# Kernel optimization log

Hardware: AMD Instinct MI355X
Metric: run time of the kernel (lower is better)

## Reference

```python
import jax, jax.numpy as jnp
import numpy as np

N = 100000
E = 800000
D_IN = 128
D_HID = 128
D_EMB = 128
D_OUT = 2


def setup_inputs() -> dict:
    key = jax.random.key(0)
    ks = jax.random.split(key, 16)
    x = jax.random.normal(ks[0], (N, D_IN), dtype=jnp.float32)
    edge_index = jax.random.randint(ks[1], (2, E), 0, N, dtype=jnp.int64)

    def lin(k, d_out, d_in, scale):
        return jax.random.normal(k, (d_out, d_in), dtype=jnp.float32) * scale

    s1 = 1.0 / np.sqrt(D_IN)
    s2 = 1.0 / np.sqrt(D_HID)
    s3 = 1.0 / np.sqrt(D_EMB)
    return {
        "x": x,
        "edge_index": edge_index,
        # layer 1: in -> hidden  (lin_l has bias, lin_r no bias, as in PyG SAGEConv)
        "Wl1": lin(ks[2], D_HID, D_IN, s1), "bl1": jnp.zeros((D_HID,), jnp.float32),
        "Wr1": lin(ks[3], D_HID, D_IN, s1),
        # layer 2: hidden -> hidden
        "Wl2": lin(ks[4], D_HID, D_HID, s2), "bl2": jnp.zeros((D_HID,), jnp.float32),
        "Wr2": lin(ks[5], D_HID, D_HID, s2),
        # layer 3: hidden -> embedding
        "Wl3": lin(ks[6], D_EMB, D_HID, s2), "bl3": jnp.zeros((D_EMB,), jnp.float32),
        "Wr3": lin(ks[7], D_EMB, D_HID, s2),
        # output head: embedding -> output (bias)
        "Wo": lin(ks[8], D_OUT, D_EMB, s3), "bo": jnp.zeros((D_OUT,), jnp.float32),
    }


def _sage_conv(x, src, dst, Wl, bl, Wr):
    # mean-aggregate neighbor (source) features onto destination nodes
    msg = x[src]                                             # [E, d]
    agg = jax.ops.segment_sum(msg, dst, num_segments=N)      # [N, d]
    deg = jax.ops.segment_sum(jnp.ones((src.shape[0],), x.dtype), dst, num_segments=N)
    agg = agg / jnp.maximum(deg, 1.0)[:, None]
    # out = lin_l(agg) + lin_r(x)
    return agg @ Wl.T + bl + x @ Wr.T


def reference(x, edge_index, Wl1, bl1, Wr1, Wl2, bl2, Wr2, Wl3, bl3, Wr3, Wo, bo):
    src, dst = edge_index[0], edge_index[1]
    h = jax.nn.relu(_sage_conv(x, src, dst, Wl1, bl1, Wr1))   # dropout is identity in eval
    h = jax.nn.relu(_sage_conv(h, src, dst, Wl2, bl2, Wr2))
    h = _sage_conv(h, src, dst, Wl3, bl3, Wr3)                # no relu on last conv
    return h @ Wo.T + bo                                      # [N, D_OUT]
```

## Files before the change

kernel.cpp:

```cpp
#include <hip/hip_runtime.h>
#include <stdint.h>

typedef unsigned int u32;
typedef unsigned short u16;
typedef __bf16 bf16x8 __attribute__((ext_vector_type(8)));
typedef float floatx4 __attribute__((ext_vector_type(4)));
typedef u32 u32x4 __attribute__((ext_vector_type(4)));
typedef float floatx4f __attribute__((ext_vector_type(4)));
typedef float floatx4v __attribute__((ext_vector_type(4)));
typedef float floatx16 __attribute__((ext_vector_type(16)));
typedef float floatx4b __attribute__((ext_vector_type(4)));
typedef float floatx4c __attribute__((ext_vector_type(4)));
typedef float floatx4d __attribute__((ext_vector_type(4)));
typedef float floatx4e __attribute__((ext_vector_type(4)));

__device__ __forceinline__ u16 f2b(float f) {
    u32 u = __builtin_bit_cast(u32, f);
    u32 r = u + 0x7FFFu + ((u >> 16) & 1u);
    return (u16)(r >> 16);
}
__device__ __forceinline__ float lo2f(u32 u) { return __builtin_bit_cast(float, u << 16); }
__device__ __forceinline__ float hi2f(u32 u) { return __builtin_bit_cast(float, u & 0xFFFF0000u); }

__device__ __forceinline__ void self_detect(const int* ei, const u32* xw, int& is64, int& isbf) {
    int lane = threadIdx.x & 63;
    int v = ei ? ei[2 * lane + 1] : 0;
    unsigned long long b1 = __ballot(v == 0);
    u32 w = xw ? xw[lane] : 0;
    u32 e = (w >> 7) & 0xFF;
    int plaus = (e == 0) || (e >= 90 && e <= 140);
    unsigned long long b2 = __ballot(plaus);
    is64 = (b1 == ~0ULL) ? 1 : 0;
    isbf = (b2 == ~0ULL) ? 1 : 0;
}

__device__ __forceinline__ float load_f(const void* __restrict__ p, int isbf, size_t i) {
    if (isbf) {
        u16 s = ((const u16*)p)[i];
        return __builtin_bit_cast(float, ((u32)s) << 16);
    }
    return ((const float*)p)[i];
}

#define CH 4096
#define CAPB 3072

__global__ __launch_bounds__(1024) void front_kernel(
    const void* __restrict__ xraw, const int* __restrict__ ei, int E, int N, int cvb,
    u32* __restrict__ xb, int* __restrict__ gcur, u32* __restrict__ csrbkt,
    const void* Wl1, const void* Wr1, const void* Wl2, const void* Wr2,
    const void* Wl3, const void* Wr3, const void* b1, const void* b2,
    const void* b3, const void* Wo, const void* bo,
    u16* __restrict__ Wcp, float* __restrict__ smalls) {
    __shared__ int lhist[1024], loff[1024], lcur[1024], gofs[1024], wsum[16];
    __shared__ u32 ebuf[CH];
    __shared__ u16 ebkt[CH];
    int blk = blockIdx.x;
    int t = threadIdx.x;

    if (blk < cvb) {
        int is64, isbf;
        self_detect(nullptr, (const u32*)xraw, is64, isbf);
        int i = blk * 1024 + t;
        int count4 = N * 16;
        if (i >= count4) return;
        if (isbf) {
            ((u32x4*)xb)[i] = ((const u32x4*)xraw)[i];
        } else {
            typedef float fx4 __attribute__((ext_vector_type(4)));
            const fx4* f4 = (const fx4*)xraw;
            fx4 f0 = f4[2 * i], f1 = f4[2 * i + 1];
            u32x4 o;
            o.x = (u32)f2b(f0.x) | ((u32)f2b(f0.y) << 16);
            o.y = (u32)f2b(f0.z) | ((u32)f2b(f0.w) << 16);
            o.z = (u32)f2b(f1.x) | ((u32)f2b(f1.y) << 16);
            o.w = (u32)f2b(f1.z) | ((u32)f2b(f1.w) << 16);
            ((u32x4*)xb)[i] = o;
        }
        return;
    }
    if (blk < cvb + 12) {
        int is64, isbf;
        self_detect(nullptr, (const u32*)xraw, is64, isbf);
        int tg = (blk - cvb) * 1024 + t;
        int l = tg >> 12;
        int tt = tg & 4095;
        const void* Wl = (l == 0) ? Wl1 : (l == 1) ? Wl2 : Wl3;
        const void* Wr = (l == 0) ? Wr1 : (l == 1) ? Wr2 : Wr3;
        u16* Wout = Wcp + (size_t)l * 32768;
        int ln = tt & 63;
        int c = tt >> 6;
        int sk = c >> 3;
        int jt = c & 7;
        int j = jt * 16 + (ln & 15);
        int kb = sk * 32 + (ln >> 4) * 8;
#pragma unroll
        for (int jj = 0; jj < 8; ++jj) {
            int k = kb + jj;
            float v = (k < 128) ? load_f(Wl, isbf, (size_t)j * 128 + k)
                                : load_f(Wr, isbf, (size_t)j * 128 + (k - 128));
            Wout[tt * 8 + jj] = f2b(v);
        }
        return;
    }
    if (blk == cvb + 12) {
        int is64, isbf;
        self_detect(nullptr, (const u32*)xraw, is64, isbf);
        if (t < 642) {
            float v;
            if (t < 128) v = load_f(b1, isbf, t);
            else if (t < 256) v = load_f(b2, isbf, t - 128);
            else if (t < 384) v = load_f(b3, isbf, t - 256);
            else if (t < 640) v = load_f(Wo, isbf, t - 384);
            else v = load_f(bo, isbf, t - 640);
            smalls[t] = v;
        }
        return;
    }

    int is64, isbf;
    self_detect(ei, nullptr, is64, isbf);
    int cbase = (blk - (cvb + 13)) * CH;
    int cn = E - cbase;
    if (cn > CH) cn = CH;
    lhist[t] = 0;
    __syncthreads();
    int mysrc[4], myb[4], mydl[4];
#pragma unroll
    for (int k = 0; k < 4; ++k) {
        int i = t + k * 1024;
        myb[k] = -1;
        if (i < cn) {
            int e = cbase + i;
            int s, d;
            if (is64) {
                s = (int)((const uint2*)ei)[(size_t)e].x;
                d = (int)((const uint2*)ei)[(size_t)E + e].x;
            } else {
                s = ei[(size_t)e];
                d = ei[(size_t)E + e];
            }
            if ((unsigned)s >= (unsigned)N) s = 0;
            if ((unsigned)d >= (unsigned)N) d = 0;
            mysrc[k] = s;
            mydl[k] = d & 255;
            myb[k] = d >> 8;
            atomicAdd(&lhist[myb[k]], 1);
        }
    }
    __syncthreads();
    int lane = t & 63, wid = t >> 6;
    int v = lhist[t];
    int inc = v;
#pragma unroll
    for (int off = 1; off < 64; off <<= 1) {
        int o = __shfl_up(inc, off);
        if (lane >= off) inc += o;
    }
    if (lane == 63) wsum[wid] = inc;
    __syncthreads();
    int wpre = 0;
    for (int w = 0; w < wid; ++w) wpre += wsum[w];
    int excl = wpre + inc - v;
    loff[t] = excl;
    lcur[t] = excl;
    if (v > 0) gofs[t] = atomicAdd(&gcur[t], v);
    __syncthreads();
#pragma unroll
    for (int k = 0; k < 4; ++k) {
        if (myb[k] >= 0) {
            int pos = atomicAdd(&lcur[myb[k]], 1);
            ebuf[pos] = (u32)mysrc[k] | ((u32)mydl[k] << 24);
            ebkt[pos] = (u16)myb[k];
        }
    }
    __syncthreads();
#pragma unroll
    for (int k = 0; k < 4; ++k) {
        int i = t + k * 1024;
        if (i < cn) {
            int bb = ebkt[i];
            int local = gofs[bb] + (i - loff[bb]);
            if (local < CAPB) csrbkt[(size_t)bb * CAPB + local] = ebuf[i];
        }
    }
}

__global__ __launch_bounds__(512) void csr_build_kernel(
    const u32* __restrict__ csrbkt, const int* __restrict__ gcur,
    int N, int* __restrict__ gtot,
    int* __restrict__ offs, int* __restrict__ cnt,
    int* __restrict__ csr) {
    __shared__ int lh[256], lcur[256], wsum[4];
    __shared__ int sbase;
    __shared__ u32 sbuf[CAPB];
    int t = threadIdx.x;
    int b = blockIdx.x;
    int cb = gcur[b];
    if (cb > CAPB) cb = CAPB;
    const u32* bsrc = csrbkt + (size_t)b * CAPB;
    int d0 = b << 8;
    if (t < 256) lh[t] = 0;
    __syncthreads();
    for (int i = t; i < cb; i += 512) atomicAdd(&lh[bsrc[i] >> 24], 1);
    __syncthreads();
    int lane = t & 63, wid = t >> 6;
    if (t < 256) {
        int v = lh[t];
        int inc = v;
#pragma unroll
        for (int off = 1; off < 64; off <<= 1) {
            int o = __shfl_up(inc, off);
            if (lane >= off) inc += o;
        }
        if (lane == 63) wsum[wid] = inc;
    }
    __syncthreads();
    if (t < 256) {
        int v = lh[t];
        int inc = v;
#pragma unroll
        for (int off = 1; off < 64; off <<= 1) {
            int o = __shfl_up(inc, off);
            if (lane >= off) inc += o;
        }
        int wpre = 0;
        for (int w = 0; w < wid; ++w) wpre += wsum[w];
        int excl = wpre + inc - v;
        lcur[t] = excl;
        int d = d0 + t;
        if (d < N) {
            lh[t] = excl;
            cnt[d] = v;
        }
    }
    if (t == 0) sbase = atomicAdd(gtot, cb);
    __syncthreads();
    int base = sbase;
    if (t < 256) {
        int d = d0 + t;
        if (d < N) offs[d] = base + lh[t];
    }
    for (int i = t; i < cb; i += 512) {
        u32 e = bsrc[i];
        int pos = atomicAdd(&lcur[e >> 24], 1);
        sbuf[pos] = e & 0xFFFFFFu;
    }
    __syncthreads();
    for (int i = t; i < cb; i += 512) csr[base + i] = (int)sbuf[i];
}


__global__ void agg_kernel(const u32* __restrict__ F2, const int* __restrict__ offs,
                           const int* __restrict__ cnt, const int* __restrict__ csr,
                           u32* __restrict__ Aout, int N, int tstride) {
    int sub = blockIdx.x / tstride;
    int tile = blockIdx.x % tstride;
    int w = threadIdx.x >> 6;
    int lane = threadIdx.x & 63;
    int nd0 = tile * 128 + sub * 16 + w * 4;
    if (nd0 >= N) return;
    int nd1 = nd0 + 4 < N ? nd0 + 4 : N;
    for (int nd = nd0; nd < nd1; ++nd) {
        int start = offs[nd];
        int num = cnt[nd];
        float a0 = 0.f, a1 = 0.f;
        int i = 0;
        for (; i + 8 <= num; i += 8) {
            int s0 = csr[start + i + 0], s1 = csr[start + i + 1];
            int s2 = csr[start + i + 2], s3 = csr[start + i + 3];
            int s4 = csr[start + i + 4], s5 = csr[start + i + 5];
            int s6 = csr[start + i + 6], s7 = csr[start + i + 7];
            u32 u0 = F2[(size_t)s0 * 64 + lane];
            u32 u1 = F2[(size_t)s1 * 64 + lane];
            u32 u2 = F2[(size_t)s2 * 64 + lane];
            u32 u3 = F2[(size_t)s3 * 64 + lane];
            u32 u4 = F2[(size_t)s4 * 64 + lane];
            u32 u5 = F2[(size_t)s5 * 64 + lane];
            u32 u6 = F2[(size_t)s6 * 64 + lane];
            u32 u7 = F2[(size_t)s7 * 64 + lane];
            a0 += lo2f(u0) + lo2f(u1) + lo2f(u2) + lo2f(u3) +
                  lo2f(u4) + lo2f(u5) + lo2f(u6) + lo2f(u7);
            a1 += hi2f(u0) + hi2f(u1) + hi2f(u2) + hi2f(u3) +
                  hi2f(u4) + hi2f(u5) + hi2f(u6) + hi2f(u7);
        }
        for (; i + 4 <= num; i += 4) {
            int s0 = csr[start + i + 0], s1 = csr[start + i + 1];
            int s2 = csr[start + i + 2], s3 = csr[start + i + 3];
            u32 u0 = F2[(size_t)s0 * 64 + lane];
            u32 u1 = F2[(size_t)s1 * 64 + lane];
            u32 u2 = F2[(size_t)s2 * 64 + lane];
            u32 u3 = F2[(size_t)s3 * 64 + lane];
            a0 += lo2f(u0) + lo2f(u1) + lo2f(u2) + lo2f(u3);
            a1 += hi2f(u0) + hi2f(u1) + hi2f(u2) + hi2f(u3);
        }
        for (; i < num; ++i) {
            u32 u = F2[(size_t)csr[start + i] * 64 + lane];
            a0 += lo2f(u);
            a1 += hi2f(u);
        }
        float sc = 1.0f / (float)(num > 1 ? num : 1);
        a0 *= sc;
        a1 *= sc;
        Aout[(size_t)nd * 64 + lane] = (u32)f2b(a0) | ((u32)f2b(a1) << 16);
    }
}

__global__ __launch_bounds__(256, 4) void gemm_kernel(
    const u32* __restrict__ aggb, u32* Fio,
    const u16* __restrict__ Wcp, const float* __restrict__ biasf,
    int N, int relu, const float* __restrict__ headw,
    const u32* __restrict__ xw, void* __restrict__ outp, int gstride) {
    __shared__ u16 ldsT[4][16][132];
    int tid = threadIdx.x;
    int w = tid >> 6;
    int lane = tid & 63;
    int r16 = lane & 15;
    int g4 = lane >> 4;
    int tile = blockIdx.x % gstride;
    int half = blockIdx.x / gstride;
    int nbase = tile * 128 + half * 64;
    if (nbase >= N) return;
    int nd0 = nbase + w * 16;
    int node = nd0 + r16;
    int nodeC = (node < N) ? node : (N - 1);
    const u32* aRow = aggb + (size_t)nodeC * 64 + g4 * 4;
    const u32* fRow = Fio + (size_t)nodeC * 64 + g4 * 4;

    floatx4 acc[8];
#pragma unroll
    for (int jt = 0; jt < 8; ++jt) acc[jt] = 0.0f;

#pragma unroll
    for (int s = 0; s < 8; ++s) {
        const u32* ap = (s < 4) ? (aRow + (size_t)s * 16) : (fRow + (size_t)(s - 4) * 16);
        bf16x8 a = *reinterpret_cast<const bf16x8*>(ap);
        const u16* bp = Wcp + (size_t)((s * 8) * 64 + lane) * 8;
#pragma unroll
        for (int jt = 0; jt < 8; ++jt) {
            bf16x8 b = *reinterpret_cast<const bf16x8*>(bp + (size_t)jt * 64 * 8);
            acc[jt] = __builtin_amdgcn_mfma_f32_16x16x32_bf16(a, b, acc[jt], 0, 0, 0);
        }
    }

    if (outp == nullptr) {
#pragma unroll
        for (int jt = 0; jt < 8; ++jt) {
            int j = jt * 16 + r16;
            float bf = biasf[j];
#pragma unroll
            for (int r = 0; r < 4; ++r) {
                float v = acc[jt][r] + bf;
                if (relu) v = fmaxf(v, 0.0f);
                ldsT[w][g4 * 4 + r][j] = f2b(v);
            }
        }
        int rowg = nd0 + r16;
        if (rowg < N) {
            u32* drow = &Fio[(size_t)rowg * 64 + g4 * 16];
#pragma unroll
            for (int i = 0; i < 4; ++i) {
                const u16* lp = &ldsT[w][r16][g4 * 32 + i * 8];
                uint2 lo = *reinterpret_cast<const uint2*>(lp);
                uint2 hi = *reinterpret_cast<const uint2*>(lp + 4);
                u32x4 o;
                o.x = lo.x; o.y = lo.y; o.z = hi.x; o.w = hi.y;
                *reinterpret_cast<u32x4*>(drow + i * 4) = o;
            }
        }
    } else {
        int is64, isbf;
        self_detect(nullptr, xw, is64, isbf);
#pragma unroll
        for (int r = 0; r < 4; ++r) {
            float p0 = 0.f, p1 = 0.f;
#pragma unroll
            for (int jt = 0; jt < 8; ++jt) {
                int j = jt * 16 + r16;
                float v = acc[jt][r] + biasf[j];
                p0 += v * headw[j];
                p1 += v * headw[128 + j];
            }
#pragma unroll
            for (int off = 8; off > 0; off >>= 1) {
                p0 += __shfl_xor(p0, off);
                p1 += __shfl_xor(p1, off);
            }
            if (r16 == 0) {
                int nodeS = nd0 + g4 * 4 + r;
                if (nodeS < N) {
                    float o0 = p0 + headw[256];
                    float o1 = p1 + headw[257];
                    if (isbf)
                        ((u32*)outp)[nodeS] = (u32)f2b(o0) | ((u32)f2b(o1) << 16);
                    else
                        ((float2*)outp)[nodeS] = make_float2(o0, o1);
                }
            }
        }
    }
}

extern "C" void kernel_launch(void* const* d_in, const int* in_sizes, int n_in,
                              void* d_out, int out_size, void* d_ws, size_t ws_size,
                              hipStream_t stream) {
    const int N = in_sizes[0] / 128;
    const int E = in_sizes[1] / 2;

    const void* x = d_in[0];
    const int* ei = (const int*)d_in[1];
    const void* Wl[3] = {d_in[2], d_in[5], d_in[8]};
    const void* bl[3] = {d_in[3], d_in[6], d_in[9]};
    const void* Wr[3] = {d_in[4], d_in[7], d_in[10]};
    const void* Wo = d_in[11];
    const void* bo = d_in[12];

    char* p = (char*)d_ws;
    auto alloc = [&](size_t bytes) -> char* {
        char* r = p;
        p += (bytes + 255) & ~(size_t)255;
        return r;
    };
    int* offs = (int*)alloc((size_t)N * 4);
    int* cnt = (int*)alloc((size_t)N * 4);
    float* smalls = (float*)alloc(642 * 4);
    int* gcur = (int*)alloc(1025 * 4);
    int* csr = (int*)alloc(((size_t)E + CAPB + 64) * 4);
    u16* Wcp = (u16*)alloc((size_t)3 * 4096 * 8 * 2);
    u32* xb = (u32*)alloc((size_t)(N + 1) * 64 * 4);
    u32* aggb = (u32*)alloc((size_t)N * 64 * 4);
    u32* csrbkt = aggb;
    int* gtot = gcur + 1024;
    (void)ws_size;

    const int NB = (N + 255) / 256;
    const int cvb = (N * 16 + 1023) / 1024;
    const int sb = (E + CH - 1) / CH;
    const int gb = (N + 127) / 128;
    const int tstride = (gb + 7) & ~7;
    const int ab = 8 * tstride;
    const int gstride = tstride;
    const int ggrid = 2 * gstride;

    hipMemsetAsync(gcur, 0, 1025 * 4, stream);
    front_kernel<<<cvb + 13 + sb, 1024, 0, stream>>>(
        x, ei, E, N, cvb, xb, gcur, csrbkt,
        Wl[0], Wr[0], Wl[1], Wr[1], Wl[2], Wr[2],
        bl[0], bl[1], bl[2], Wo, bo, Wcp, smalls);
    csr_build_kernel<<<NB, 512, 0, stream>>>(csrbkt, gcur, N, gtot, offs, cnt, csr);

    agg_kernel<<<ab, 256, 0, stream>>>(xb, offs, cnt, csr, aggb, N, tstride);
    gemm_kernel<<<ggrid, 256, 0, stream>>>(aggb, xb, Wcp, smalls, N, 1, nullptr, nullptr, nullptr, gstride);
    agg_kernel<<<ab, 256, 0, stream>>>(xb, offs, cnt, csr, aggb, N, tstride);
    gemm_kernel<<<ggrid, 256, 0, stream>>>(aggb, xb, Wcp + 32768, smalls + 128, N, 1, nullptr, nullptr, nullptr, gstride);
    agg_kernel<<<ab, 256, 0, stream>>>(xb, offs, cnt, csr, aggb, N, tstride);
    gemm_kernel<<<ggrid, 256, 0, stream>>>(aggb, xb, Wcp + 65536, smalls + 256, N, 0,
                                           smalls + 384, (const u32*)x, d_out, gstride);
}
```

Before: 342.4 us.

## Fuse neighbor aggregation and SAGE GEMM into one per-layer kernel

Merges the separate aggregation and MFMA GEMM kernels into one layer kernel. Each block aggregates 16 nodes into shared memory, then runs the 16x128 GEMM from LDS, with each wave computing 32 output columns. Node features now ping-pong between two buffers, so a layer never overwrites its own input. This removes the aggregate buffer round trip through global memory and three kernel launches. The cost is a much smaller GEMM tile per block, weights re-read per 16 nodes, and extra barriers plus shared atomics in the head reduction.

```diff
diff --git a/kernel.cpp b/kernel.cpp
--- a/kernel.cpp
+++ b/kernel.cpp
@@ -6,13 +6,6 @@
 typedef __bf16 bf16x8 __attribute__((ext_vector_type(8)));
 typedef float floatx4 __attribute__((ext_vector_type(4)));
 typedef u32 u32x4 __attribute__((ext_vector_type(4)));
-typedef float floatx4f __attribute__((ext_vector_type(4)));
-typedef float floatx4v __attribute__((ext_vector_type(4)));
-typedef float floatx16 __attribute__((ext_vector_type(16)));
-typedef float floatx4b __attribute__((ext_vector_type(4)));
-typedef float floatx4c __attribute__((ext_vector_type(4)));
-typedef float floatx4d __attribute__((ext_vector_type(4)));
-typedef float floatx4e __attribute__((ext_vector_type(4)));
 
 __device__ __forceinline__ u16 f2b(float f) {
     u32 u = __builtin_bit_cast(u32, f);
@@ -250,16 +243,25 @@
     for (int i = t; i < cb; i += 512) csr[base + i] = (int)sbuf[i];
 }
 
-
-__global__ void agg_kernel(const u32* __restrict__ F2, const int* __restrict__ offs,
-                           const int* __restrict__ cnt, const int* __restrict__ csr,
-                           u32* __restrict__ Aout, int N, int tstride) {
+__global__ __launch_bounds__(256) void layer_kernel(
+    const u32* __restrict__ xcur, u32* __restrict__ xnxt,
+    const int* __restrict__ offs, const int* __restrict__ cnt,
+    const int* __restrict__ csr,
+    const u16* __restrict__ Wcp, const float* __restrict__ biasf,
+    int N, int relu, const float* __restrict__ headw,
+    const u32* __restrict__ xw, void* __restrict__ outp, int tstride) {
+    __shared__ u32 aggL[16][68];
+    __shared__ float hsum[16][2];
     int sub = blockIdx.x / tstride;
     int tile = blockIdx.x % tstride;
-    int w = threadIdx.x >> 6;
-    int lane = threadIdx.x & 63;
-    int nd0 = tile * 128 + sub * 16 + w * 4;
-    if (nd0 >= N) return;
+    int t = threadIdx.x;
+    int w = t >> 6;
+    int lane = t & 63;
+    int nd0b = tile * 128 + sub * 16;
+    if (nd0b >= N) return;
+    if (t < 32) ((float*)hsum)[t] = 0.f;
+
+    int nd0 = nd0b + w * 4;
     int nd1 = nd0 + 4 < N ? nd0 + 4 : N;
     for (int nd = nd0; nd < nd1; ++nd) {
         int start = offs[nd];
@@ -271,14 +273,14 @@
             int s2 = csr[start + i + 2], s3 = csr[start + i + 3];
             int s4 = csr[start + i + 4], s5 = csr[start + i + 5];
             int s6 = csr[start + i + 6], s7 = csr[start + i + 7];
-            u32 u0 = F2[(size_t)s0 * 64 + lane];
-            u32 u1 = F2[(size_t)s1 * 64 + lane];
-            u32 u2 = F2[(size_t)s2 * 64 + lane];
-            u32 u3 = F2[(size_t)s3 * 64 + lane];
-            u32 u4 = F2[(size_t)s4 * 64 + lane];
-            u32 u5 = F2[(size_t)s5 * 64 + lane];
-            u32 u6 = F2[(size_t)s6 * 64 + lane];
-            u32 u7 = F2[(size_t)s7 * 64 + lane];
+            u32 u0 = xcur[(size_t)s0 * 64 + lane];
+            u32 u1 = xcur[(size_t)s1 * 64 + lane];
+            u32 u2 = xcur[(size_t)s2 * 64 + lane];
+            u32 u3 = xcur[(size_t)s3 * 64 + lane];
+            u32 u4 = xcur[(size_t)s4 * 64 + lane];
+            u32 u5 = xcur[(size_t)s5 * 64 + lane];
+            u32 u6 = xcur[(size_t)s6 * 64 + lane];
+            u32 u7 = xcur[(size_t)s7 * 64 + lane];
             a0 += lo2f(u0) + lo2f(u1) + lo2f(u2) + lo2f(u3) +
                   lo2f(u4) + lo2f(u5) + lo2f(u6) + lo2f(u7);
             a1 += hi2f(u0) + hi2f(u1) + hi2f(u2) + hi2f(u3) +
@@ -287,115 +289,106 @@
         for (; i + 4 <= num; i += 4) {
             int s0 = csr[start + i + 0], s1 = csr[start + i + 1];
             int s2 = csr[start + i + 2], s3 = csr[start + i + 3];
-            u32 u0 = F2[(size_t)s0 * 64 + lane];
-            u32 u1 = F2[(size_t)s1 * 64 + lane];
-            u32 u2 = F2[(size_t)s2 * 64 + lane];
-            u32 u3 = F2[(size_t)s3 * 64 + lane];
+            u32 u0 = xcur[(size_t)s0 * 64 + lane];
+            u32 u1 = xcur[(size_t)s1 * 64 + lane];
+            u32 u2 = xcur[(size_t)s2 * 64 + lane];
+            u32 u3 = xcur[(size_t)s3 * 64 + lane];
             a0 += lo2f(u0) + lo2f(u1) + lo2f(u2) + lo2f(u3);
             a1 += hi2f(u0) + hi2f(u1) + hi2f(u2) + hi2f(u3);
         }
         for (; i < num; ++i) {
-            u32 u = F2[(size_t)csr[start + i] * 64 + lane];
+            u32 u = xcur[(size_t)csr[start + i] * 64 + lane];
             a0 += lo2f(u);
             a1 += hi2f(u);
         }
         float sc = 1.0f / (float)(num > 1 ? num : 1);
         a0 *= sc;
         a1 *= sc;
-        Aout[(size_t)nd * 64 + lane] = (u32)f2b(a0) | ((u32)f2b(a1) << 16);
-    }
-}
-
-__global__ __launch_bounds__(256, 4) void gemm_kernel(
-    const u32* __restrict__ aggb, u32* Fio,
-    const u16* __restrict__ Wcp, const float* __restrict__ biasf,
-    int N, int relu, const float* __restrict__ headw,
-    const u32* __restrict__ xw, void* __restrict__ outp, int gstride) {
-    __shared__ u16 ldsT[4][16][132];
-    int tid = threadIdx.x;
-    int w = tid >> 6;
-    int lane = tid & 63;
+        aggL[nd - nd0b][lane] = (u32)f2b(a0) | ((u32)f2b(a1) << 16);
+    }
+    __syncthreads();
+
     int r16 = lane & 15;
     int g4 = lane >> 4;
-    int tile = blockIdx.x % gstride;
-    int half = blockIdx.x / gstride;
-    int nbase = tile * 128 + half * 64;
-    if (nbase >= N) return;
-    int nd0 = nbase + w * 16;
-    int node = nd0 + r16;
-    int nodeC = (node < N) ? node : (N - 1);
-    const u32* aRow = aggb + (size_t)nodeC * 64 + g4 * 4;
-    const u32* fRow = Fio + (size_t)nodeC * 64 + g4 * 4;
-
-    floatx4 acc[8];
-#pragma unroll
-    for (int jt = 0; jt < 8; ++jt) acc[jt] = 0.0f;
-
+    int noder = nd0b + r16;
+    int nodeC = (noder < N) ? noder : (N - 1);
+    floatx4 acc0 = 0.0f, acc1 = 0.0f;
+    const u16* bbase = Wcp + (size_t)lane * 8 + (size_t)(w * 2) * 512;
 #pragma unroll
     for (int s = 0; s < 8; ++s) {
-        const u32* ap = (s < 4) ? (aRow + (size_t)s * 16) : (fRow + (size_t)(s - 4) * 16);
-        bf16x8 a = *reinterpret_cast<const bf16x8*>(ap);
-        const u16* bp = Wcp + (size_t)((s * 8) * 64 + lane) * 8;
-#pragma unroll
-        for (int jt = 0; jt < 8; ++jt) {
-            bf16x8 b = *reinterpret_cast<const bf16x8*>(bp + (size_t)jt * 64 * 8);
-            acc[jt] = __builtin_amdgcn_mfma_f32_16x16x32_bf16(a, b, acc[jt], 0, 0, 0);
-        }
-    }
+        bf16x8 a;
+        if (s < 4) {
+            a = *reinterpret_cast<const bf16x8*>(&aggL[r16][s * 16 + g4 * 4]);
+        } else {
+            a = *reinterpret_cast<const bf16x8*>(
+                xcur + (size_t)nodeC * 64 + (s - 4) * 16 + g4 * 4);
+        }
+        const u16* bp = bbase + (size_t)(s * 8) * 512;
+        bf16x8 b0 = *reinterpret_cast<const bf16x8*>(bp);
+        bf16x8 b1 = *reinterpret_cast<const bf16x8*>(bp + 512);
+        acc0 = __builtin_amdgcn_mfma_f32_16x16x32_bf16(a, b0, acc0, 0, 0, 0);
+        acc1 = __builtin_amdgcn_mfma_f32_16x16x32_bf16(a, b1, acc1, 0, 0, 0);
+    }
+    __syncthreads();
 
     if (outp == nullptr) {
-#pragma unroll
-        for (int jt = 0; jt < 8; ++jt) {
-            int j = jt * 16 + r16;
-            float bf = biasf[j];
-#pragma unroll
-            for (int r = 0; r < 4; ++r) {
-                float v = acc[jt][r] + bf;
-                if (relu) v = fmaxf(v, 0.0f);
-                ldsT[w][g4 * 4 + r][j] = f2b(v);
-            }
-        }
-        int rowg = nd0 + r16;
-        if (rowg < N) {
-            u32* drow = &Fio[(size_t)rowg * 64 + g4 * 16];
-#pragma unroll
-            for (int i = 0; i < 4; ++i) {
-                const u16* lp = &ldsT[w][r16][g4 * 32 + i * 8];
-                uint2 lo = *reinterpret_cast<const uint2*>(lp);
-                uint2 hi = *reinterpret_cast<const uint2*>(lp + 4);
-                u32x4 o;
-                o.x = lo.x; o.y = lo.y; o.z = hi.x; o.w = hi.y;
-                *reinterpret_cast<u32x4*>(drow + i * 4) = o;
-            }
+        u16* ldsO = (u16*)aggL;
+        int col0 = w * 32 + r16;
+        float bf0 = biasf[col0], bf1 = biasf[col0 + 16];
+#pragma unroll
+        for (int r = 0; r < 4; ++r) {
+            int row = g4 * 4 + r;
+            float v0 = acc0[r] + bf0;
+            float v1 = acc1[r] + bf1;
+            if (relu) { v0 = fmaxf(v0, 0.0f); v1 = fmaxf(v1, 0.0f); }
+            ldsO[row * 136 + col0] = f2b(v0);
+            ldsO[row * 136 + col0 + 16] = f2b(v1);
+        }
+        __syncthreads();
+        int row = t >> 4, seg = t & 15;
+        int nodeS = nd0b + row;
+        if (nodeS < N) {
+            const u16* lp = ldsO + row * 136 + seg * 8;
+            uint2 lo = *reinterpret_cast<const uint2*>(lp);
+            uint2 hi = *reinterpret_cast<const uint2*>(lp + 4);
+            u32x4 o;
+            o.x = lo.x; o.y = lo.y; o.z = hi.x; o.w = hi.y;
+            *reinterpret_cast<u32x4*>(&xnxt[(size_t)nodeS * 64 + seg * 4]) = o;
         }
     } else {
         int is64, isbf;
         self_detect(nullptr, xw, is64, isbf);
+        int col0 = w * 32 + r16;
+        int col1 = col0 + 16;
+        float bf0 = biasf[col0], bf1 = biasf[col1];
+        float w00 = headw[col0], w01 = headw[col1];
+        float w10 = headw[128 + col0], w11 = headw[128 + col1];
 #pragma unroll
         for (int r = 0; r < 4; ++r) {
-            float p0 = 0.f, p1 = 0.f;
-#pragma unroll
-            for (int jt = 0; jt < 8; ++jt) {
-                int j = jt * 16 + r16;
-                float v = acc[jt][r] + biasf[j];
-                p0 += v * headw[j];
-                p1 += v * headw[128 + j];
-            }
+            float h0 = acc0[r] + bf0;
+            float h1 = acc1[r] + bf1;
+            float p0 = h0 * w00 + h1 * w01;
+            float p1 = h0 * w10 + h1 * w11;
 #pragma unroll
             for (int off = 8; off > 0; off >>= 1) {
                 p0 += __shfl_xor(p0, off);
                 p1 += __shfl_xor(p1, off);
             }
             if (r16 == 0) {
-                int nodeS = nd0 + g4 * 4 + r;
-                if (nodeS < N) {
-                    float o0 = p0 + headw[256];
-                    float o1 = p1 + headw[257];
-                    if (isbf)
-                        ((u32*)outp)[nodeS] = (u32)f2b(o0) | ((u32)f2b(o1) << 16);
-                    else
-                        ((float2*)outp)[nodeS] = make_float2(o0, o1);
-                }
+                atomicAdd(&hsum[g4 * 4 + r][0], p0);
+                atomicAdd(&hsum[g4 * 4 + r][1], p1);
+            }
+        }
+        __syncthreads();
+        if (t < 16) {
+            int nodeS = nd0b + t;
+            if (nodeS < N) {
+                float o0 = hsum[t][0] + headw[256];
+                float o1 = hsum[t][1] + headw[257];
+                if (isbf)
+                    ((u32*)outp)[nodeS] = (u32)f2b(o0) | ((u32)f2b(o1) << 16);
+                else
+                    ((float2*)outp)[nodeS] = make_float2(o0, o1);
             }
         }
     }
@@ -427,9 +420,9 @@
     int* gcur = (int*)alloc(1025 * 4);
     int* csr = (int*)alloc(((size_t)E + CAPB + 64) * 4);
     u16* Wcp = (u16*)alloc((size_t)3 * 4096 * 8 * 2);
-    u32* xb = (u32*)alloc((size_t)(N + 1) * 64 * 4);
-    u32* aggb = (u32*)alloc((size_t)N * 64 * 4);
-    u32* csrbkt = aggb;
+    u32* x0 = (u32*)alloc((size_t)(N + 1) * 64 * 4);
+    u32* x1 = (u32*)alloc((size_t)(N + 1) * 64 * 4);
+    u32* csrbkt = x1;
     int* gtot = gcur + 1024;
     (void)ws_size;
 
@@ -439,21 +432,18 @@
     const int gb = (N + 127) / 128;
     const int tstride = (gb + 7) & ~7;
     const int ab = 8 * tstride;
-    const int gstride = tstride;
-    const int ggrid = 2 * gstride;
 
     hipMemsetAsync(gcur, 0, 1025 * 4, stream);
     front_kernel<<<cvb + 13 + sb, 1024, 0, stream>>>(
-        x, ei, E, N, cvb, xb, gcur, csrbkt,
+        x, ei, E, N, cvb, x0, gcur, csrbkt,
         Wl[0], Wr[0], Wl[1], Wr[1], Wl[2], Wr[2],
         bl[0], bl[1], bl[2], Wo, bo, Wcp, smalls);
     csr_build_kernel<<<NB, 512, 0, stream>>>(csrbkt, gcur, N, gtot, offs, cnt, csr);
 
-    agg_kernel<<<ab, 256, 0, stream>>>(xb, offs, cnt, csr, aggb, N, tstride);
-    gemm_kernel<<<ggrid, 256, 0, stream>>>(aggb, xb, Wcp, smalls, N, 1, nullptr, nullptr, nullptr, gstride);
-    agg_kernel<<<ab, 256, 0, stream>>>(xb, offs, cnt, csr, aggb, N, tstride);
-    gemm_kernel<<<ggrid, 256, 0, stream>>>(aggb, xb, Wcp + 32768, smalls + 128, N, 1, nullptr, nullptr, nullptr, gstride);
-    agg_kernel<<<ab, 256, 0, stream>>>(xb, offs, cnt, csr, aggb, N, tstride);
-    gemm_kernel<<<ggrid, 256, 0, stream>>>(aggb, xb, Wcp + 65536, smalls + 256, N, 0,
-                                           smalls + 384, (const u32*)x, d_out, gstride);
-}
+    layer_kernel<<<ab, 256, 0, stream>>>(x0, x1, offs, cnt, csr, Wcp, smalls, N, 1,
+                                         nullptr, nullptr, nullptr, tstride);
+    layer_kernel<<<ab, 256, 0, stream>>>(x1, x0, offs, cnt, csr, Wcp + 32768, smalls + 128, N, 1,
+                                         nullptr, nullptr, nullptr, tstride);
+    layer_kernel<<<ab, 256, 0, stream>>>(x0, x1, offs, cnt, csr, Wcp + 65536, smalls + 256, N, 0,
+                                         smalls + 384, (const u32*)x, d_out, tstride);
+}
```

After: 325.8 us. 1.05x faster.
